# Kernel tuning notes

Hardware: AMD Instinct MI355X
Metric: run time of the kernel (lower is better)

## Reference

```python
import jax, jax.numpy as jnp
import numpy as np

N, E, M = 4096, 65536, 16   # nodes, edges, channel multiplicity per degree
MID = 32                    # RadialFunc hidden width (SE3-Transformer default)
EPS = 1e-5                  # BatchNorm1d eps
DEGS = [0, 1]
PAIRS = [(0, 0), (0, 1), (1, 0), (1, 1)]  # (d_in, d_out)


def _bn_relu(x, g, b):
    # BatchNorm1d in training mode (biased batch stats over edges) + ReLU
    mu = x.mean(0, keepdims=True)
    var = ((x - mu) ** 2).mean(0, keepdims=True)
    return jax.nn.relu((x - mu) / jnp.sqrt(var + EPS) * g + b)


def _radial(feat, w1, b1, g1, be1, w2, b2, g2, be2, w3, b3, nf):
    # RadialFunc: Linear-BN-ReLU, Linear-BN-ReLU, Linear -> [E, nc_out, 1, nc_in, 1, nf]
    y = _bn_relu(feat @ w1 + b1, g1, be1)
    y = _bn_relu(y @ w2 + b2, g2, be2)
    y = y @ w3 + b3
    return y.reshape(-1, M, 1, M, 1, nf)


def _forward(h0, h1, r, basis00, basis01, basis10, basis11,
             rw1, rb1, rg1, rbe1, rw2, rb2, rg2, rbe2,
             w3_00, b3_00, w3_01, b3_01, w3_10, b3_10, w3_11, b3_11,
             Wself0, Wself1, edge_src, edge_dst):
    h = {0: h0, 1: h1}
    basis = {(0, 0): basis00, (0, 1): basis01, (1, 0): basis10, (1, 1): basis11}
    w3b3 = {(0, 0): (w3_00, b3_00), (0, 1): (w3_01, b3_01),
            (1, 0): (w3_10, b3_10), (1, 1): (w3_11, b3_11)}
    Wself = {0: Wself0, 1: Wself1}
    # PairwiseConv: per-edge kernel = sum_f R * basis  -> [E, M, 2do+1, M, 2di+1]
    kern = {}
    for p, (di, do) in enumerate(PAIRS):
        nf = 2 * min(di, do) + 1
        w3, b3 = w3b3[(di, do)]
        R = _radial(r, rw1[p], rb1[p], rg1[p], rbe1[p],
                    rw2[p], rb2[p], rg2[p], rbe2[p], w3, b3, nf)
        kern[(di, do)] = (R * basis[(di, do)]).sum(-1)
    cnt = jnp.maximum(
        jax.ops.segment_sum(jnp.ones((E,), h0.dtype), edge_dst, num_segments=N), 1.0)
    outs = []
    for do in DEGS:
        msg = jnp.zeros((E, M, 2 * do + 1), h0.dtype)
        for di in DEGS:
            # per-edge small matmul: kernel @ gathered source feature
            msg = msg + jnp.einsum('eopiq,eiq->eop', kern[(di, do)], h[di][edge_src])
        # self-interaction, flavor='skip': add W @ destination feature per edge
        msg = msg + jnp.einsum('mi,eip->emp', Wself[do][0], h[do][edge_dst])
        s = jax.ops.segment_sum(msg, edge_dst, num_segments=N)  # scatter-mean
        outs.append(s / cnt[:, None, None])
    return tuple(outs)


def setup_inputs() -> dict:
    key = jax.random.key(0)
    ks = jax.random.split(key, 20)
    nrm = lambda k, sh, s=1.0: jax.random.normal(k, sh, jnp.float32) * s
    return {
        'h0': nrm(ks[0], (N, M, 1)),
        'h1': nrm(ks[1], (N, M, 3)),
        'r': jax.random.uniform(ks[2], (E, 1), jnp.float32),
        'basis00': nrm(ks[3], (E, 1, 1, 1, 1, 1)),
        'basis01': nrm(ks[4], (E, 1, 3, 1, 1, 1)),
        'basis10': nrm(ks[5], (E, 1, 1, 1, 3, 1)),
        'basis11': nrm(ks[6], (E, 1, 3, 1, 3, 3)),
        'rw1': nrm(ks[7], (4, 1, MID)),
        'rb1': jnp.zeros((4, MID), jnp.float32),
        'rg1': jnp.ones((4, MID), jnp.float32),
        'rbe1': jnp.zeros((4, MID), jnp.float32),
        'rw2': nrm(ks[8], (4, MID, MID), 1.0 / np.sqrt(MID)),
        'rb2': jnp.zeros((4, MID), jnp.float32),
        'rg2': jnp.ones((4, MID), jnp.float32),
        'rbe2': jnp.zeros((4, MID), jnp.float32),
        'w3_00': nrm(ks[9], (MID, M * M), 1.0 / np.sqrt(MID)),
        'b3_00': jnp.zeros((M * M,), jnp.float32),
        'w3_01': nrm(ks[10], (MID, M * M), 1.0 / np.sqrt(MID)),
        'b3_01': jnp.zeros((M * M,), jnp.float32),
        'w3_10': nrm(ks[11], (MID, M * M), 1.0 / np.sqrt(MID)),
        'b3_10': jnp.zeros((M * M,), jnp.float32),
        'w3_11': nrm(ks[12], (MID, M * M * 3), 1.0 / np.sqrt(MID)),
        'b3_11': jnp.zeros((M * M * 3,), jnp.float32),
        'Wself0': nrm(ks[13], (1, M, M), 1.0 / np.sqrt(M)),
        'Wself1': nrm(ks[14], (1, M, M), 1.0 / np.sqrt(M)),
        'edge_src': jax.random.randint(ks[15], (E,), 0, N),
        'edge_dst': jax.random.randint(ks[16], (E,), 0, N),
    }


def reference(h0, h1, r, basis00, basis01, basis10, basis11,
              rw1, rb1, rg1, rbe1, rw2, rb2, rg2, rbe2,
              w3_00, b3_00, w3_01, b3_01, w3_10, b3_10, w3_11, b3_11,
              Wself0, Wself1, edge_src, edge_dst):
    return _forward(h0, h1, r, basis00, basis01, basis10, basis11,
                    rw1, rb1, rg1, rbe1, rw2, rb2, rg2, rbe2,
                    w3_00, b3_00, w3_01, b3_01, w3_10, b3_10, w3_11, b3_11,
                    Wself0, Wself1, edge_src, edge_dst)
```

## Files before the change

kernel.cpp:

```cpp
#include <hip/hip_runtime.h>

#define N_NODES 4096
#define N_EDGES 65536
#define MID 32
#define BN_EPS 1e-5f

#define WS_RSUM    0
#define WS_RSUMSQ  1
#define WS_ALPHA1  272
#define WS_BETA1   400
#define WS_A2      528
#define WS_S2      656
#define WS_GRAM    5120
#define WS_SUMY    9216
#define WS_W2T     17664
#define WS_MSG_F   262144
#define WS_U00     4456448
#define WS_U01     4521984
#define WS_V10     4587520
#define WS_W11     4784128
#define WS_DEG_I   1024
#define WS_CUR_I   9344
#define WS_OFFS_I  13440
#define WS_ELIST_I 65536
#define WSB_WA     524288
#define WSB_WB     557056
#define WSB_WC     573440

typedef short bf16x8 __attribute__((ext_vector_type(8)));
typedef float f32x4  __attribute__((ext_vector_type(4)));

__device__ __forceinline__ unsigned short f2bf(float x) {
    unsigned u = __float_as_uint(x);
    u += 0x7fffu + ((u >> 16) & 1u);
    return (unsigned short)(u >> 16);
}

__device__ __forceinline__ int wimg_idx(int col, int k) {
    return col * 32 + ((((col >> 1) + (k >> 3)) & 3) << 3) + (k & 7);
}

__global__ void __launch_bounds__(256) k_pre(const float* __restrict__ rw2,
        const float* __restrict__ w300, const float* __restrict__ w301,
        const float* __restrict__ w310, const float* __restrict__ w311,
        const float* __restrict__ bw300, const float* __restrict__ bw301,
        const float* __restrict__ bw310, const float* __restrict__ bw311,
        const float* __restrict__ r, const int* __restrict__ edst,
        const float* __restrict__ h0, const float* __restrict__ h1,
        float* __restrict__ wsf) {
    if (blockIdx.x < 128) {
        int t = blockIdx.x * 256 + threadIdx.x;
        char* wsb = (char*)wsf;
        if (t < 4096) {
            int p = t >> 10, rem = t & 1023, c = rem >> 5, k = rem & 31;
            wsf[WS_W2T + t] = rw2[(p << 10) + (k << 5) + c];
        }
        if (t < 16384) {
            int col = t >> 5, k = t & 31;
            float v = (col < 256) ? w300[(k << 8) + col] : w310[(k << 8) + (col - 256)];
            ((unsigned short*)(wsb + WSB_WA))[wimg_idx(col, k)] = f2bf(v);
        }
        if (t < 8192) {
            int col = t >> 5, k = t & 31;
            ((unsigned short*)(wsb + WSB_WB))[wimg_idx(col, k)] = f2bf(w301[(k << 8) + col]);
        }
        if (t < 24576) {
            int col = t >> 5, k = t & 31;
            int f = col >> 8, rem = col & 255;
            ((unsigned short*)(wsb + WSB_WC))[wimg_idx(col, k)] = f2bf(w311[k * 768 + rem * 3 + f]);
        }
    } else if (blockIdx.x < 384) {
        int e = (blockIdx.x - 128) * 256 + threadIdx.x;
        float v = r[e];
        atomicAdd(((int*)wsf) + WS_DEG_I + edst[e], 1);
        float s = v, ss = v * v;
#pragma unroll
        for (int mk = 32; mk >= 1; mk >>= 1) {
            s  += __shfl_xor(s,  mk, 64);
            ss += __shfl_xor(ss, mk, 64);
        }
        __shared__ float ls[4], lss[4];
        int lane = threadIdx.x & 63, wv = threadIdx.x >> 6;
        if (lane == 0) { ls[wv] = s; lss[wv] = ss; }
        __syncthreads();
        if (threadIdx.x == 0) {
            atomicAdd(wsf + WS_RSUM,   ls[0] + ls[1] + ls[2] + ls[3]);
            atomicAdd(wsf + WS_RSUMSQ, lss[0] + lss[1] + lss[2] + lss[3]);
        }
    } else {
        int g = (blockIdx.x - 384) * 256 + threadIdx.x;
        int n = g >> 4, mo = g & 15;
        float h1r[48];
#pragma unroll
        for (int j = 0; j < 48; ++j) h1r[j] = h1[n * 48 + j];
        float s00 = 0.f, s01 = 0.f;
#pragma unroll
        for (int mi = 0; mi < 16; ++mi) {
            float hv = h0[n * 16 + mi];
            s00 += bw300[mo * 16 + mi] * hv;
            s01 += bw301[mo * 16 + mi] * hv;
        }
        wsf[WS_U00 + n * 16 + mo] = s00;
        wsf[WS_U01 + n * 16 + mo] = s01;
#pragma unroll
        for (int q = 0; q < 3; ++q) {
            float sv = 0.f;
#pragma unroll
            for (int mi = 0; mi < 16; ++mi)
                sv += bw310[mo * 16 + mi] * h1r[mi * 3 + q];
            wsf[WS_V10 + n * 48 + q * 16 + mo] = sv;
        }
#pragma unroll
        for (int f = 0; f < 3; ++f)
#pragma unroll
            for (int q = 0; q < 3; ++q) {
                float sv = 0.f;
#pragma unroll
                for (int mi = 0; mi < 16; ++mi)
                    sv += bw311[(mo * 16 + mi) * 3 + f] * h1r[mi * 3 + q];
                wsf[WS_W11 + n * 144 + (f * 3 + q) * 16 + mo] = sv;
            }
    }
}

__global__ void __launch_bounds__(512) k_gram(const float* __restrict__ r,
        const float* __restrict__ rw1, const float* __restrict__ rg1,
        const float* __restrict__ rbe1, float* __restrict__ wsf) {
    int t = threadIdx.x;
    int wv = t >> 6, lane = t & 63;
    int quad = lane >> 4, lq = lane & 15;
    int p  = __builtin_amdgcn_readfirstlane(wv & 3);
    int mt = __builtin_amdgcn_readfirstlane(wv >> 2);
    float mu_r  = wsf[WS_RSUM] * (1.f / N_EDGES);
    float var_r = wsf[WS_RSUMSQ] * (1.f / N_EDGES) - mu_r * mu_r;
    float al[2], be[2];
#pragma unroll
    for (int hh = 0; hh < 2; ++hh) {
        int ch = p * 32 + hh * 16 + lq;
        float w1 = rw1[ch];
        float a = w1 * rg1[ch] * rsqrtf(w1 * w1 * var_r + BN_EPS);
        al[hh] = a;
        be[hh] = rbe1[ch] - a * mu_r;
    }
    bf16x8 ones;
#pragma unroll
    for (int j = 0; j < 8; ++j) ones[j] = (short)0x3F80;
    f32x4 accG0 = {0.f, 0.f, 0.f, 0.f};
    f32x4 accG1 = {0.f, 0.f, 0.f, 0.f};
    f32x4 accS  = {0.f, 0.f, 0.f, 0.f};
    int ebase = blockIdx.x * 512;
#pragma unroll 1
    for (int ks = 0; ks < 16; ++ks) {
        const float* rp = r + ebase + ks * 32 + quad * 8;
        float4 ra = *(const float4*)(rp);
        float4 rb = *(const float4*)(rp + 4);
        float rv[8] = {ra.x, ra.y, ra.z, ra.w, rb.x, rb.y, rb.z, rb.w};
        bf16x8 fr0, fr1;
#pragma unroll
        for (int j = 0; j < 8; ++j) {
            fr0[j] = (short)f2bf(fmaxf(0.f, al[0] * rv[j] + be[0]));
            fr1[j] = (short)f2bf(fmaxf(0.f, al[1] * rv[j] + be[1]));
        }
        bf16x8 fA = mt ? fr1 : fr0;
        accG0 = __builtin_amdgcn_mfma_f32_16x16x32_bf16(fA, fr0, accG0, 0, 0, 0);
        accG1 = __builtin_amdgcn_mfma_f32_16x16x32_bf16(fA, fr1, accG1, 0, 0, 0);
        accS  = __builtin_amdgcn_mfma_f32_16x16x32_bf16(fA, ones, accS,  0, 0, 0);
    }
    float* G = wsf + WS_GRAM + p * 1024;
#pragma unroll
    for (int reg = 0; reg < 4; ++reg) {
        int k1 = mt * 16 + quad * 4 + reg;
        atomicAdd(&G[k1 * 32 + lq],      accG0[reg]);
        atomicAdd(&G[k1 * 32 + 16 + lq], accG1[reg]);
    }
    if (lq == 0) {
#pragma unroll
        for (int reg = 0; reg < 4; ++reg)
            atomicAdd(wsf + WS_SUMY + p * 32 + mt * 16 + quad * 4 + reg, accS[reg]);
    }
}

__global__ void __launch_bounds__(1024) k_fs(const float* __restrict__ rw1,
        const float* __restrict__ rg1, const float* __restrict__ rbe1,
        const float* __restrict__ rg2, const float* __restrict__ rbe2,
        const float* __restrict__ rb2, float* __restrict__ wsf) {
    int t = threadIdx.x;
    if (t < 128) {
        float mu_r  = wsf[WS_RSUM] * (1.f / N_EDGES);
        float var_r = wsf[WS_RSUMSQ] * (1.f / N_EDGES) - mu_r * mu_r;
        float w1 = rw1[t];
        float al = w1 * rg1[t] * rsqrtf(w1 * w1 * var_r + BN_EPS);
        wsf[WS_ALPHA1 + t] = al;
        wsf[WS_BETA1  + t] = rbe1[t] - al * mu_r;
        int p = t >> 5, c = t & 31;
        const float* G = wsf + WS_GRAM + p * 1024;
        const float* w = wsf + WS_W2T + p * 1024 + c * 32;
        float invE = 1.f / N_EDGES;
        float s1 = 0.f;
#pragma unroll 1
        for (int k = 0; k < 32; ++k) s1 += w[k] * (wsf[WS_SUMY + p * 32 + k] * invE);
        float q = 0.f;
#pragma unroll 1
        for (int k1 = 0; k1 < 32; ++k1) {
            float a = 0.f;
#pragma unroll
            for (int k2 = 0; k2 < 32; ++k2) a += w[k2] * G[k1 * 32 + k2];
            q += w[k1] * a;
        }
        float var = q * invE - s1 * s1;
        float a2 = rg2[t] * rsqrtf(var + BN_EPS);
        wsf[WS_A2 + t] = a2;
        float mu2 = rb2[t] + s1;
        wsf[WS_S2 + t] = rbe2[t] - mu2 * a2;
    }
    __shared__ int sdata[1024];
    const int* deg = ((const int*)wsf) + WS_DEG_I;
    int* offs = ((int*)wsf) + WS_OFFS_I;
    int* cur  = ((int*)wsf) + WS_CUR_I;
    int v0 = deg[t * 4], v1 = deg[t * 4 + 1], v2 = deg[t * 4 + 2], v3 = deg[t * 4 + 3];
    sdata[t] = v0 + v1 + v2 + v3;
    __syncthreads();
    for (int off = 1; off < 1024; off <<= 1) {
        int x = sdata[t];
        int y = (t >= off) ? sdata[t - off] : 0;
        __syncthreads();
        sdata[t] = x + y;
        __syncthreads();
    }
    int excl = (t == 0) ? 0 : sdata[t - 1];
    int o0 = excl, o1 = excl + v0, o2 = o1 + v1, o3 = o2 + v2;
    offs[t * 4] = o0;     cur[t * 4] = o0;
    offs[t * 4 + 1] = o1; cur[t * 4 + 1] = o1;
    offs[t * 4 + 2] = o2; cur[t * 4 + 2] = o2;
    offs[t * 4 + 3] = o3; cur[t * 4 + 3] = o3;
    if (t == 1023) offs[4096] = sdata[1023];
}

__global__ void __launch_bounds__(256) k_cb(const int* __restrict__ edst,
        const float* __restrict__ b00, const float* __restrict__ b01,
        const float* __restrict__ b10, const float* __restrict__ b11,
        const int* __restrict__ esrc, float* __restrict__ wsf,
        float* __restrict__ msg) {
    if (blockIdx.x < 256) {
        int e = blockIdx.x * 256 + threadIdx.x;
        int d = edst[e];
        int* cur   = ((int*)wsf) + WS_CUR_I;
        int* elist = ((int*)wsf) + WS_ELIST_I;
        int pos = atomicAdd(&cur[d], 1);
        elist[pos] = e;
        return;
    }
    int g = (blockIdx.x - 256) * 256 + threadIdx.x;
    int e = g >> 2, quad = g & 3;
    int s = esrc[e];
    float4 u00q = *(const float4*)(wsf + WS_U00 + s * 16 + quad * 4);
    float b00v = b00[e];
    float m0[4];
#pragma unroll
    for (int rr = 0; rr < 4; ++rr) m0[rr] = b00v * ((const float*)&u00q)[rr];
#pragma unroll
    for (int q = 0; q < 3; ++q) {
        float4 vq = *(const float4*)(wsf + WS_V10 + s * 48 + q * 16 + quad * 4);
        float bq = b10[e * 3 + q];
#pragma unroll
        for (int rr = 0; rr < 4; ++rr) m0[rr] += bq * ((const float*)&vq)[rr];
    }
    {
        float4 w = {m0[0], m0[1], m0[2], m0[3]};
        *(float4*)(msg + (size_t)e * 64 + quad * 4) = w;
    }
    float4 u01q = *(const float4*)(wsf + WS_U01 + s * 16 + quad * 4);
    float bo0 = b01[e * 3 + 0], bo1 = b01[e * 3 + 1], bo2 = b01[e * 3 + 2];
    float m1[4][3];
#pragma unroll
    for (int rr = 0; rr < 4; ++rr) {
        float u = ((const float*)&u01q)[rr];
        m1[rr][0] = bo0 * u; m1[rr][1] = bo1 * u; m1[rr][2] = bo2 * u;
    }
#pragma unroll
    for (int f = 0; f < 3; ++f)
#pragma unroll
        for (int q = 0; q < 3; ++q) {
            float4 wq = *(const float4*)(wsf + WS_W11 + s * 144 + (f * 3 + q) * 16 + quad * 4);
#pragma unroll
            for (int o = 0; o < 3; ++o) {
                float bas = b11[e * 27 + o * 9 + q * 3 + f];
#pragma unroll
                for (int rr = 0; rr < 4; ++rr) m1[rr][o] += bas * ((const float*)&wq)[rr];
            }
        }
    float* base = msg + (size_t)e * 64 + 16 + quad * 12;
    float4 w0 = {m1[0][0], m1[0][1], m1[0][2], m1[1][0]};
    float4 w1 = {m1[1][1], m1[1][2], m1[2][0], m1[2][1]};
    float4 w2 = {m1[2][2], m1[3][0], m1[3][1], m1[3][2]};
    *(float4*)(base)     = w0;
    *(float4*)(base + 4) = w1;
    *(float4*)(base + 8) = w2;
}

__device__ __forceinline__ void y2_lds16(int p, int el, int c0, float rv,
                                         const float* __restrict__ wsf,
                                         const float* __restrict__ rb2, char* dst) {
    float y1[MID];
#pragma unroll
    for (int k = 0; k < MID; ++k)
        y1[k] = fmaxf(0.f, wsf[WS_ALPHA1 + p * 32 + k] * rv + wsf[WS_BETA1 + p * 32 + k]);
    unsigned short h[16];
#pragma unroll
    for (int cc = 0; cc < 16; ++cc) {
        int c = c0 + cc;
        float x = rb2[p * 32 + c];
#pragma unroll
        for (int k = 0; k < MID; ++k) x += y1[k] * wsf[WS_W2T + p * 1024 + c * 32 + k];
        h[cc] = f2bf(fmaxf(0.f, wsf[WS_A2 + p * 32 + c] * x + wsf[WS_S2 + p * 32 + c]));
    }
#pragma unroll
    for (int q = 0; q < 2; ++q) {
        int4 pk;
        pk.x = (int)h[q * 8 + 0] | ((int)h[q * 8 + 1] << 16);
        pk.y = (int)h[q * 8 + 2] | ((int)h[q * 8 + 3] << 16);
        pk.z = (int)h[q * 8 + 4] | ((int)h[q * 8 + 5] << 16);
        pk.w = (int)h[q * 8 + 6] | ((int)h[q * 8 + 7] << 16);
        int jc = (c0 >> 3) + q;
        int slot = ((el >> 1) + jc) & 3;
        *(int4*)(dst + el * 64 + slot * 16) = pk;
    }
}

__global__ void __launch_bounds__(512, 2) k_msg(const float* __restrict__ r,
        const float* __restrict__ h0, const float* __restrict__ h1,
        const float* __restrict__ b00, const float* __restrict__ b01,
        const float* __restrict__ b10, const float* __restrict__ b11,
        const float* __restrict__ rb2,
        const int* __restrict__ esrc,
        const float* __restrict__ wsf, float* __restrict__ msg) {
    extern __shared__ char smem[];
    short* w3s = (short*)smem;
    const char* wsb = (const char*)wsf;
    int t = threadIdx.x;
    int wv = t >> 6, lane = t & 63;
    int quad = lane >> 4, lq = lane & 15;
    int eb = blockIdx.x << 8;
    int woff = (((lq >> 1) + quad) & 3) << 3;
    int yoff = (((lq >> 1) + quad) & 3) << 4;

    {
        const float4* src = (const float4*)(wsb + WSB_WA);
        float4* dst = (float4*)smem;
#pragma unroll
        for (int i = 0; i < 4; ++i) dst[i * 512 + t] = src[i * 512 + t];
    }
    {
        int p = __builtin_amdgcn_readfirstlane((t >> 8) * 2);
        int el = t & 255;
        float rv = r[eb + el];
        char* dst = smem + 32768 + (t >> 8) * 16384;
        y2_lds16(p, el, 0, rv, wsf, rb2, dst);
        y2_lds16(p, el, 16, rv, wsf, rb2, dst);
    }
    __syncthreads();
#pragma unroll
    for (int g2 = 0; g2 < 2; ++g2) {
        int el = (wv * 2 + g2) * 16 + lq;
        int e = eb + el;
        int s = esrc[e];
        bf16x8 bf0 = *(const bf16x8*)(smem + 32768 + el * 64 + yoff);
        bf16x8 bf2 = *(const bf16x8*)(smem + 49152 + el * 64 + yoff);
        float4 h0q = *(const float4*)(h0 + s * 16 + quad * 4);
        float4 hv0 = *(const float4*)(h1 + s * 48 + quad * 12);
        float4 hv1 = *(const float4*)(h1 + s * 48 + quad * 12 + 4);
        float4 hv2 = *(const float4*)(h1 + s * 48 + quad * 12 + 8);
        float b00v = b00[e];
        float bq0 = b10[e * 3 + 0], bq1 = b10[e * 3 + 1], bq2 = b10[e * 3 + 2];
        float gq0 = bq0 * hv0.x + bq1 * hv0.y + bq2 * hv0.z;
        float gq1 = bq0 * hv0.w + bq1 * hv1.x + bq2 * hv1.y;
        float gq2 = bq0 * hv1.z + bq1 * hv1.w + bq2 * hv2.x;
        float gq3 = bq0 * hv2.y + bq1 * hv2.z + bq2 * hv2.w;
        float4 a0v = *(const float4*)(msg + (size_t)e * 64 + quad * 4);
        float a0[4] = {a0v.x, a0v.y, a0v.z, a0v.w};
#pragma unroll
        for (int m = 0; m < 16; ++m) {
            bf16x8 af = *(const bf16x8*)(w3s + (m * 16 + lq) * 32 + woff);
            f32x4 dd = __builtin_amdgcn_mfma_f32_16x16x32_bf16(af, bf0, (f32x4){0.f,0.f,0.f,0.f}, 0, 0, 0);
            float partial = dd[0] * h0q.x + dd[1] * h0q.y + dd[2] * h0q.z + dd[3] * h0q.w;
            partial += __shfl_xor(partial, 16);
            partial += __shfl_xor(partial, 32);
            a0[m & 3] += (quad == (m >> 2)) ? b00v * partial : 0.f;
        }
#pragma unroll
        for (int m = 0; m < 16; ++m) {
            bf16x8 af = *(const bf16x8*)(w3s + (256 + m * 16 + lq) * 32 + woff);
            f32x4 dd = __builtin_amdgcn_mfma_f32_16x16x32_bf16(af, bf2, (f32x4){0.f,0.f,0.f,0.f}, 0, 0, 0);
            float partial = dd[0] * gq0 + dd[1] * gq1 + dd[2] * gq2 + dd[3] * gq3;
            partial += __shfl_xor(partial, 16);
            partial += __shfl_xor(partial, 32);
            a0[m & 3] += (quad == (m >> 2)) ? partial : 0.f;
        }
        float4 w = {a0[0], a0[1], a0[2], a0[3]};
        *(float4*)(msg + (size_t)e * 64 + quad * 4) = w;
    }
    __syncthreads();

    {
        const float4* src = (const float4*)(wsb + WSB_WB);
        float4* dst = (float4*)smem;
#pragma unroll
        for (int i = 0; i < 2; ++i) dst[i * 512 + t] = src[i * 512 + t];
    }
    {
        int el = t & 255, c0 = (t >> 8) * 16;
        y2_lds16(1, el, c0, r[eb + el], wsf, rb2, smem + 16384);
    }
    __syncthreads();
#pragma unroll
    for (int g2 = 0; g2 < 2; ++g2) {
        int el = (wv * 2 + g2) * 16 + lq;
        int e = eb + el;
        int s = esrc[e];
        bf16x8 bf1 = *(const bf16x8*)(smem + 16384 + el * 64 + yoff);
        float4 h0q = *(const float4*)(h0 + s * 16 + quad * 4);
        float d1[4] = {0.f, 0.f, 0.f, 0.f};
#pragma unroll
        for (int m = 0; m < 16; ++m) {
            bf16x8 af = *(const bf16x8*)(w3s + (m * 16 + lq) * 32 + woff);
            f32x4 dd = __builtin_amdgcn_mfma_f32_16x16x32_bf16(af, bf1, (f32x4){0.f,0.f,0.f,0.f}, 0, 0, 0);
            float partial = dd[0] * h0q.x + dd[1] * h0q.y + dd[2] * h0q.z + dd[3] * h0q.w;
            partial += __shfl_xor(partial, 16);
            partial += __shfl_xor(partial, 32);
            d1[m & 3] += (quad == (m >> 2)) ? partial : 0.f;
        }
        float bo0 = b01[e * 3 + 0], bo1 = b01[e * 3 + 1], bo2 = b01[e * 3 + 2];
        float* base = msg + (size_t)e * 64 + 16 + quad * 12;
        float4 r0 = *(const float4*)(base);
        float4 r1 = *(const float4*)(base + 4);
        float4 r2 = *(const float4*)(base + 8);
        float4 w0 = {r0.x + bo0 * d1[0], r0.y + bo1 * d1[0], r0.z + bo2 * d1[0], r0.w + bo0 * d1[1]};
        float4 w1 = {r1.x + bo1 * d1[1], r1.y + bo2 * d1[1], r1.z + bo0 * d1[2], r1.w + bo1 * d1[2]};
        float4 w2 = {r2.x + bo2 * d1[2], r2.y + bo0 * d1[3], r2.z + bo1 * d1[3], r2.w + bo2 * d1[3]};
        *(float4*)(base)     = w0;
        *(float4*)(base + 4) = w1;
        *(float4*)(base + 8) = w2;
    }
    __syncthreads();

    {
        const float4* src = (const float4*)(wsb + WSB_WC);
        float4* dst = (float4*)smem;
#pragma unroll
        for (int i = 0; i < 6; ++i) dst[i * 512 + t] = src[i * 512 + t];
    }
    {
        int el = t & 255, c0 = (t >> 8) * 16;
        y2_lds16(3, el, c0, r[eb + el], wsf, rb2, smem + 49152);
    }
    __syncthreads();
#pragma unroll
    for (int g2 = 0; g2 < 2; ++g2) {
        int el = (wv * 2 + g2) * 16 + lq;
        int e = eb + el;
        int s = esrc[e];
        bf16x8 bf3 = *(const bf16x8*)(smem + 49152 + el * 64 + yoff);
        float4 hv0 = *(const float4*)(h1 + s * 48 + quad * 12);
        float4 hv1 = *(const float4*)(h1 + s * 48 + quad * 12 + 4);
        float4 hv2 = *(const float4*)(h1 + s * 48 + quad * 12 + 8);
        float h1v[4][3] = {{hv0.x, hv0.y, hv0.z}, {hv0.w, hv1.x, hv1.y},
                           {hv1.z, hv1.w, hv2.x}, {hv2.y, hv2.z, hv2.w}};
        float m1[4][3];
#pragma unroll
        for (int rr = 0; rr < 4; ++rr)
#pragma unroll
            for (int o = 0; o < 3; ++o) m1[rr][o] = 0.f;
#pragma unroll
        for (int f = 0; f < 3; ++f) {
            float Tf[4][3];
#pragma unroll
            for (int o = 0; o < 3; ++o) {
                float bv0 = b11[e * 27 + o * 9 + 0 + f];
                float bv1 = b11[e * 27 + o * 9 + 3 + f];
                float bv2 = b11[e * 27 + o * 9 + 6 + f];
#pragma unroll
                for (int rr = 0; rr < 4; ++rr)
                    Tf[rr][o] = h1v[rr][0] * bv0 + h1v[rr][1] * bv1 + h1v[rr][2] * bv2;
            }
#pragma unroll
            for (int m = 0; m < 16; ++m) {
                int colb = f * 256 + m * 16 + lq;
                bf16x8 af = *(const bf16x8*)(w3s + colb * 32 + woff);
                f32x4 dd = __builtin_amdgcn_mfma_f32_16x16x32_bf16(af, bf3, (f32x4){0.f,0.f,0.f,0.f}, 0, 0, 0);
#pragma unroll
                for (int o = 0; o < 3; ++o) {
                    float po = dd[0] * Tf[0][o] + dd[1] * Tf[1][o] + dd[2] * Tf[2][o] + dd[3] * Tf[3][o];
                    po += __shfl_xor(po, 16);
                    po += __shfl_xor(po, 32);
                    m1[m & 3][o] += (quad == (m >> 2)) ? po : 0.f;
                }
            }
        }
        float* base = msg + (size_t)e * 64 + 16 + quad * 12;
        float4 r0 = *(const float4*)(base);
        float4 r1 = *(const float4*)(base + 4);
        float4 r2 = *(const float4*)(base + 8);
        float4 w0 = {m1[0][0] + r0.x, m1[0][1] + r0.y, m1[0][2] + r0.z, m1[1][0] + r0.w};
        float4 w1 = {m1[1][1] + r1.x, m1[1][2] + r1.y, m1[2][0] + r1.z, m1[2][1] + r1.w};
        float4 w2 = {m1[2][2] + r2.x, m1[3][0] + r2.y, m1[3][1] + r2.z, m1[3][2] + r2.w};
        *(float4*)(base)     = w0;
        *(float4*)(base + 4) = w1;
        *(float4*)(base + 8) = w2;
    }
}

__global__ void __launch_bounds__(256) k_gather(const float* __restrict__ h0,
        const float* __restrict__ h1, const float* __restrict__ Wself0,
        const float* __restrict__ Wself1, const float* __restrict__ wsf,
        float* __restrict__ out) {
    int wv = threadIdx.x >> 6, lane = threadIdx.x & 63;
    int n = blockIdx.x * 4 + wv;
    const int* offs  = ((const int*)wsf) + WS_OFFS_I;
    const int* elist = ((const int*)wsf) + WS_ELIST_I;
    const float* msg = wsf + WS_MSG_F;
    int start = offs[n], end = offs[n + 1];
    int deg = end - start;
    float acc = 0.f;
    for (int j0 = 0; j0 < deg; j0 += 64) {
        int cnt = min(64, deg - j0);
        int eidv = (j0 + lane < deg) ? elist[start + j0 + lane] : 0;
        int jj = 0;
        for (; jj + 3 < cnt; jj += 4) {
            int e0 = __shfl(eidv, jj), e1 = __shfl(eidv, jj + 1);
            int e2 = __shfl(eidv, jj + 2), e3 = __shfl(eidv, jj + 3);
            float v0 = msg[(size_t)e0 * 64 + lane];
            float v1 = msg[(size_t)e1 * 64 + lane];
            float v2 = msg[(size_t)e2 * 64 + lane];
            float v3 = msg[(size_t)e3 * 64 + lane];
            acc += (v0 + v1) + (v2 + v3);
        }
        for (; jj < cnt; ++jj) {
            int eid = __shfl(eidv, jj);
            acc += msg[(size_t)eid * 64 + lane];
        }
    }
    float self = 0.f;
    if (lane < 16) {
        int m = lane;
#pragma unroll
        for (int i = 0; i < 16; ++i) self += Wself0[m * 16 + i] * h0[n * 16 + i];
    } else {
        int idx = lane - 16; int m = idx / 3, o = idx % 3;
#pragma unroll
        for (int i = 0; i < 16; ++i) self += Wself1[m * 16 + i] * h1[n * 48 + i * 3 + o];
    }
    float c = (float)(deg > 0 ? deg : 1);
    float res = acc / c + (deg > 0 ? self : 0.f);
    if (lane < 16) out[n * 16 + lane] = res;
    else           out[65536 + n * 48 + (lane - 16)] = res;
}

extern "C" void kernel_launch(void* const* d_in, const int* in_sizes, int n_in,
                              void* d_out, int out_size, void* d_ws, size_t ws_size,
                              hipStream_t stream) {
    const float* h0   = (const float*)d_in[0];
    const float* h1   = (const float*)d_in[1];
    const float* r    = (const float*)d_in[2];
    const float* b00  = (const float*)d_in[3];
    const float* b01  = (const float*)d_in[4];
    const float* b10  = (const float*)d_in[5];
    const float* b11  = (const float*)d_in[6];
    const float* rw1  = (const float*)d_in[7];
    const float* rg1  = (const float*)d_in[9];
    const float* rbe1 = (const float*)d_in[10];
    const float* rw2  = (const float*)d_in[11];
    const float* rb2  = (const float*)d_in[12];
    const float* rg2  = (const float*)d_in[13];
    const float* rbe2 = (const float*)d_in[14];
    const float* w300 = (const float*)d_in[15];
    const float* bw300= (const float*)d_in[16];
    const float* w301 = (const float*)d_in[17];
    const float* bw301= (const float*)d_in[18];
    const float* w310 = (const float*)d_in[19];
    const float* bw310= (const float*)d_in[20];
    const float* w311 = (const float*)d_in[21];
    const float* bw311= (const float*)d_in[22];
    const float* Wself0 = (const float*)d_in[23];
    const float* Wself1 = (const float*)d_in[24];
    const int* esrc = (const int*)d_in[25];
    const int* edst = (const int*)d_in[26];
    float* out = (float*)d_out;
    float* wsf = (float*)d_ws;
    float* msg = wsf + WS_MSG_F;

    static bool attr_set = false;
    if (!attr_set) {
        hipFuncSetAttribute((const void*)k_msg,
                            hipFuncAttributeMaxDynamicSharedMemorySize, 65536);
        attr_set = true;
    }

    hipMemsetAsync(d_ws, 0, 37376, stream);

    k_pre<<<640, 256, 0, stream>>>(rw2, w300, w301, w310, w311,
                                   bw300, bw301, bw310, bw311, r, edst, h0, h1, wsf);
    k_gram<<<128, 512, 0, stream>>>(r, rw1, rg1, rbe1, wsf);
    k_fs<<<1, 1024, 0, stream>>>(rw1, rg1, rbe1, rg2, rbe2, rb2, wsf);
    k_cb<<<1280, 256, 0, stream>>>(edst, b00, b01, b10, b11, esrc, wsf, msg);
    k_msg<<<256, 512, 65536, stream>>>(r, h0, h1, b00, b01, b10, b11, rb2,
                                       esrc, wsf, msg);
    k_gather<<<1024, 256, 0, stream>>>(h0, h1, Wself0, Wself1, wsf, out);
}
```

Before: 249.8 us.

## Fuse basis-combination and edge bucketing into the message kernel

Removes the separate k_cb kernel. Its per-edge combination of precomputed U00/V10/U01/W11 node terms with the basis now runs inside k_msg, which initialises the accumulators directly instead of reading back a partially written msg buffer. The destination-bucketing atomics move into extra trailing blocks of the k_msg launch. This cuts a kernel launch and a full write-then-read round trip of the per-edge message buffer. The cost is more register pressure and serial loops in k_msg, and the bucketing blocks still reserve 64 KB of LDS each.

```diff
diff --git a/kernel.cpp b/kernel.cpp
--- a/kernel.cpp
+++ b/kernel.cpp
@@ -236,68 +236,6 @@
     if (t == 1023) offs[4096] = sdata[1023];
 }
 
-__global__ void __launch_bounds__(256) k_cb(const int* __restrict__ edst,
-        const float* __restrict__ b00, const float* __restrict__ b01,
-        const float* __restrict__ b10, const float* __restrict__ b11,
-        const int* __restrict__ esrc, float* __restrict__ wsf,
-        float* __restrict__ msg) {
-    if (blockIdx.x < 256) {
-        int e = blockIdx.x * 256 + threadIdx.x;
-        int d = edst[e];
-        int* cur   = ((int*)wsf) + WS_CUR_I;
-        int* elist = ((int*)wsf) + WS_ELIST_I;
-        int pos = atomicAdd(&cur[d], 1);
-        elist[pos] = e;
-        return;
-    }
-    int g = (blockIdx.x - 256) * 256 + threadIdx.x;
-    int e = g >> 2, quad = g & 3;
-    int s = esrc[e];
-    float4 u00q = *(const float4*)(wsf + WS_U00 + s * 16 + quad * 4);
-    float b00v = b00[e];
-    float m0[4];
-#pragma unroll
-    for (int rr = 0; rr < 4; ++rr) m0[rr] = b00v * ((const float*)&u00q)[rr];
-#pragma unroll
-    for (int q = 0; q < 3; ++q) {
-        float4 vq = *(const float4*)(wsf + WS_V10 + s * 48 + q * 16 + quad * 4);
-        float bq = b10[e * 3 + q];
-#pragma unroll
-        for (int rr = 0; rr < 4; ++rr) m0[rr] += bq * ((const float*)&vq)[rr];
-    }
-    {
-        float4 w = {m0[0], m0[1], m0[2], m0[3]};
-        *(float4*)(msg + (size_t)e * 64 + quad * 4) = w;
-    }
-    float4 u01q = *(const float4*)(wsf + WS_U01 + s * 16 + quad * 4);
-    float bo0 = b01[e * 3 + 0], bo1 = b01[e * 3 + 1], bo2 = b01[e * 3 + 2];
-    float m1[4][3];
-#pragma unroll
-    for (int rr = 0; rr < 4; ++rr) {
-        float u = ((const float*)&u01q)[rr];
-        m1[rr][0] = bo0 * u; m1[rr][1] = bo1 * u; m1[rr][2] = bo2 * u;
-    }
-#pragma unroll
-    for (int f = 0; f < 3; ++f)
-#pragma unroll
-        for (int q = 0; q < 3; ++q) {
-            float4 wq = *(const float4*)(wsf + WS_W11 + s * 144 + (f * 3 + q) * 16 + quad * 4);
-#pragma unroll
-            for (int o = 0; o < 3; ++o) {
-                float bas = b11[e * 27 + o * 9 + q * 3 + f];
-#pragma unroll
-                for (int rr = 0; rr < 4; ++rr) m1[rr][o] += bas * ((const float*)&wq)[rr];
-            }
-        }
-    float* base = msg + (size_t)e * 64 + 16 + quad * 12;
-    float4 w0 = {m1[0][0], m1[0][1], m1[0][2], m1[1][0]};
-    float4 w1 = {m1[1][1], m1[1][2], m1[2][0], m1[2][1]};
-    float4 w2 = {m1[2][2], m1[3][0], m1[3][1], m1[3][2]};
-    *(float4*)(base)     = w0;
-    *(float4*)(base + 4) = w1;
-    *(float4*)(base + 8) = w2;
-}
-
 __device__ __forceinline__ void y2_lds16(int p, int el, int c0, float rv,
                                          const float* __restrict__ wsf,
                                          const float* __restrict__ rb2, char* dst) {
@@ -332,9 +270,16 @@
         const float* __restrict__ b00, const float* __restrict__ b01,
         const float* __restrict__ b10, const float* __restrict__ b11,
         const float* __restrict__ rb2,
-        const int* __restrict__ esrc,
+        const int* __restrict__ esrc, const int* __restrict__ edst,
         const float* __restrict__ wsf, float* __restrict__ msg) {
     extern __shared__ char smem[];
+    if (blockIdx.x >= 256) {
+        int e = (blockIdx.x - 256) * 512 + threadIdx.x;
+        int d = edst[e];
+        int pos = atomicAdd(((int*)wsf) + WS_CUR_I + d, 1);
+        (((int*)wsf) + WS_ELIST_I)[pos] = e;
+        return;
+    }
     short* w3s = (short*)smem;
     const char* wsb = (const char*)wsf;
     int t = threadIdx.x;
@@ -376,8 +321,14 @@
         float gq1 = bq0 * hv0.w + bq1 * hv1.x + bq2 * hv1.y;
         float gq2 = bq0 * hv1.z + bq1 * hv1.w + bq2 * hv2.x;
         float gq3 = bq0 * hv2.y + bq1 * hv2.z + bq2 * hv2.w;
-        float4 a0v = *(const float4*)(msg + (size_t)e * 64 + quad * 4);
-        float a0[4] = {a0v.x, a0v.y, a0v.z, a0v.w};
+        float4 u00q = *(const float4*)(wsf + WS_U00 + s * 16 + quad * 4);
+        float a0[4] = {b00v * u00q.x, b00v * u00q.y, b00v * u00q.z, b00v * u00q.w};
+#pragma unroll 1
+        for (int q = 0; q < 3; ++q) {
+            float4 vq = *(const float4*)(wsf + WS_V10 + s * 48 + q * 16 + quad * 4);
+            float bq = (q == 0) ? bq0 : ((q == 1) ? bq1 : bq2);
+            a0[0] += bq * vq.x; a0[1] += bq * vq.y; a0[2] += bq * vq.z; a0[3] += bq * vq.w;
+        }
 #pragma unroll
         for (int m = 0; m < 16; ++m) {
             bf16x8 af = *(const bf16x8*)(w3s + (m * 16 + lq) * 32 + woff);
@@ -419,7 +370,8 @@
         int s = esrc[e];
         bf16x8 bf1 = *(const bf16x8*)(smem + 16384 + el * 64 + yoff);
         float4 h0q = *(const float4*)(h0 + s * 16 + quad * 4);
-        float d1[4] = {0.f, 0.f, 0.f, 0.f};
+        float4 u01q = *(const float4*)(wsf + WS_U01 + s * 16 + quad * 4);
+        float d1[4] = {u01q.x, u01q.y, u01q.z, u01q.w};
 #pragma unroll
         for (int m = 0; m < 16; ++m) {
             bf16x8 af = *(const bf16x8*)(w3s + (m * 16 + lq) * 32 + woff);
@@ -430,13 +382,30 @@
             d1[m & 3] += (quad == (m >> 2)) ? partial : 0.f;
         }
         float bo0 = b01[e * 3 + 0], bo1 = b01[e * 3 + 1], bo2 = b01[e * 3 + 2];
+        float m1[4][3];
+#pragma unroll
+        for (int rr = 0; rr < 4; ++rr) {
+            m1[rr][0] = bo0 * d1[rr];
+            m1[rr][1] = bo1 * d1[rr];
+            m1[rr][2] = bo2 * d1[rr];
+        }
+#pragma unroll 1
+        for (int f = 0; f < 3; ++f)
+#pragma unroll 1
+            for (int q = 0; q < 3; ++q) {
+                float4 wq = *(const float4*)(wsf + WS_W11 + s * 144 + (f * 3 + q) * 16 + quad * 4);
+                float ba0 = b11[e * 27 + 0 * 9 + q * 3 + f];
+                float ba1 = b11[e * 27 + 1 * 9 + q * 3 + f];
+                float ba2 = b11[e * 27 + 2 * 9 + q * 3 + f];
+                m1[0][0] += ba0 * wq.x; m1[0][1] += ba1 * wq.x; m1[0][2] += ba2 * wq.x;
+                m1[1][0] += ba0 * wq.y; m1[1][1] += ba1 * wq.y; m1[1][2] += ba2 * wq.y;
+                m1[2][0] += ba0 * wq.z; m1[2][1] += ba1 * wq.z; m1[2][2] += ba2 * wq.z;
+                m1[3][0] += ba0 * wq.w; m1[3][1] += ba1 * wq.w; m1[3][2] += ba2 * wq.w;
+            }
         float* base = msg + (size_t)e * 64 + 16 + quad * 12;
-        float4 r0 = *(const float4*)(base);
-        float4 r1 = *(const float4*)(base + 4);
-        float4 r2 = *(const float4*)(base + 8);
-        float4 w0 = {r0.x + bo0 * d1[0], r0.y + bo1 * d1[0], r0.z + bo2 * d1[0], r0.w + bo0 * d1[1]};
-        float4 w1 = {r1.x + bo1 * d1[1], r1.y + bo2 * d1[1], r1.z + bo0 * d1[2], r1.w + bo1 * d1[2]};
-        float4 w2 = {r2.x + bo2 * d1[2], r2.y + bo0 * d1[3], r2.z + bo1 * d1[3], r2.w + bo2 * d1[3]};
+        float4 w0 = {m1[0][0], m1[0][1], m1[0][2], m1[1][0]};
+        float4 w1 = {m1[1][1], m1[1][2], m1[2][0], m1[2][1]};
+        float4 w2 = {m1[2][2], m1[3][0], m1[3][1], m1[3][2]};
         *(float4*)(base)     = w0;
         *(float4*)(base + 4) = w1;
         *(float4*)(base + 8) = w2;
@@ -601,8 +570,7 @@
                                    bw300, bw301, bw310, bw311, r, edst, h0, h1, wsf);
     k_gram<<<128, 512, 0, stream>>>(r, rw1, rg1, rbe1, wsf);
     k_fs<<<1, 1024, 0, stream>>>(rw1, rg1, rbe1, rg2, rbe2, rb2, wsf);
-    k_cb<<<1280, 256, 0, stream>>>(edst, b00, b01, b10, b11, esrc, wsf, msg);
-    k_msg<<<256, 512, 65536, stream>>>(r, h0, h1, b00, b01, b10, b11, rb2,
-                                       esrc, wsf, msg);
+    k_msg<<<384, 512, 65536, stream>>>(r, h0, h1, b00, b01, b10, b11, rb2,
+                                       esrc, edst, wsf, msg);
     k_gather<<<1024, 256, 0, stream>>>(h0, h1, Wself0, Wself1, wsf, out);
 }
```

Result: slower. 269.4 us (+7.8%).
